# Kernel optimization log

Measured on AMD Instinct MI355X. Metric: run time of the kernel, lower is better.

Reference implementation:

```python
import jax, jax.numpy as jnp
import numpy as np

E = 512   # fusion_dim
H = 8     # num_heads
HD = E // H
NC = 6

def _ln(x, g, b, eps=1e-5):
    m = jnp.mean(x, axis=-1, keepdims=True)
    v = jnp.mean((x - m) ** 2, axis=-1, keepdims=True)
    return (x - m) * jax.lax.rsqrt(v + eps) * g + b

def _lin(x, w, b):
    # torch nn.Linear: w is (out, in)
    return x @ w.T + b

def setup_inputs() -> dict:
    key = jax.random.key(0)
    ks = iter(jax.random.split(key, 32))
    B = 16384
    d = {
        'rgb':  jax.random.normal(next(ks), (B, 768), jnp.float32),
        'pose': jax.random.normal(next(ks), (B, 640), jnp.float32),
        'flow': jax.random.normal(next(ks), (B, 1024), jnp.float32),
    }
    def W(k, shape):
        return jax.random.normal(k, shape, jnp.float32) * 0.02
    # projection branches: Linear + LayerNorm
    d['rgb_w'] = W(next(ks), (E, 768));  d['rgb_b'] = jnp.zeros((E,))
    d['rgb_g'] = jnp.ones((E,));         d['rgb_beta'] = jnp.zeros((E,))
    d['pose_w'] = W(next(ks), (E, 640)); d['pose_b'] = jnp.zeros((E,))
    d['pose_g'] = jnp.ones((E,));        d['pose_beta'] = jnp.zeros((E,))
    d['flow_w'] = W(next(ks), (E, 1024)); d['flow_b'] = jnp.zeros((E,))
    d['flow_g'] = jnp.ones((E,));        d['flow_beta'] = jnp.zeros((E,))
    # MultiheadAttention packed qkv + out proj (torch layout)
    d['in_w'] = W(next(ks), (3 * E, E)); d['in_b'] = jnp.zeros((3 * E,))
    d['out_w'] = W(next(ks), (E, E));    d['out_b'] = jnp.zeros((E,))
    # gate MLP
    d['gw1'] = W(next(ks), (E, 3 * E)); d['gb1'] = jnp.zeros((E,))
    d['gw2'] = W(next(ks), (3, E));     d['gb2'] = jnp.zeros((3,))
    # classifier
    d['cw1'] = W(next(ks), (E // 2, E)); d['cb1'] = jnp.zeros((E // 2,))
    d['cg'] = jnp.ones((E // 2,));       d['cbeta'] = jnp.zeros((E // 2,))
    d['cw2'] = W(next(ks), (NC, E // 2)); d['cb2'] = jnp.zeros((NC,))
    return d

def _forward(rgb, pose, flow, rgb_w, rgb_b, rgb_g, rgb_beta,
             pose_w, pose_b, pose_g, pose_beta,
             flow_w, flow_b, flow_g, flow_beta,
             in_w, in_b, out_w, out_b,
             gw1, gb1, gw2, gb2,
             cw1, cb1, cg, cbeta, cw2, cb2):
    # per-modality projection: Linear -> LN -> ReLU (dropout = identity, eval mode)
    r = jax.nn.relu(_ln(_lin(rgb, rgb_w, rgb_b), rgb_g, rgb_beta))
    p = jax.nn.relu(_ln(_lin(pose, pose_w, pose_b), pose_g, pose_beta))
    f = jax.nn.relu(_ln(_lin(flow, flow_w, flow_b), flow_g, flow_beta))
    stacked = jnp.stack([r, p, f], axis=1)                 # (B, 3, E)
    # self-attention over the 3 modality tokens
    qkv = stacked @ in_w.T + in_b                          # (B, 3, 3E)
    q, k, v = jnp.split(qkv, 3, axis=-1)
    B = stacked.shape[0]
    q = q.reshape(B, 3, H, HD); k = k.reshape(B, 3, H, HD); v = v.reshape(B, 3, H, HD)
    scores = jnp.einsum('bqhd,bkhd->bhqk', q, k) / np.sqrt(HD).astype(np.float32)
    attn = jax.nn.softmax(scores, axis=-1)
    ctx = jnp.einsum('bhqk,bkhd->bqhd', attn, v).reshape(B, 3, E)
    attended = ctx @ out_w.T + out_b                       # (B, 3, E)
    # gating over concatenated projections
    concat = jnp.concatenate([r, p, f], axis=1)            # (B, 3E)
    gate = jax.nn.softmax(_lin(jax.nn.relu(_lin(concat, gw1, gb1)), gw2, gb2), axis=1)  # (B, 3)
    fused = jnp.einsum('bse,bs->be', attended, gate)       # (B, E)
    # classifier
    h = jax.nn.relu(_ln(_lin(fused, cw1, cb1), cg, cbeta))
    logits = _lin(h, cw2, cb2)                             # (B, NC)
    return logits, gate

def reference(rgb, pose, flow, rgb_w, rgb_b, rgb_g, rgb_beta,
              pose_w, pose_b, pose_g, pose_beta,
              flow_w, flow_b, flow_g, flow_beta,
              in_w, in_b, out_w, out_b,
              gw1, gb1, gw2, gb2,
              cw1, cb1, cg, cbeta, cw2, cb2):
    return _forward(rgb, pose, flow, rgb_w, rgb_b, rgb_g, rgb_beta,
                    pose_w, pose_b, pose_g, pose_beta,
                    flow_w, flow_b, flow_g, flow_beta,
                    in_w, in_b, out_w, out_b,
                    gw1, gb1, gw2, gb2,
                    cw1, cb1, cg, cbeta, cw2, cb2)
```

## Files before the change

### kernel.cpp

```cpp
#include <hip/hip_runtime.h>


typedef unsigned short u16;
typedef __bf16 bf16x8 __attribute__((ext_vector_type(8)));
typedef float f32x4  __attribute__((ext_vector_type(4)));
typedef unsigned short u16x8 __attribute__((ext_vector_type(8)));
typedef unsigned short u16x4 __attribute__((ext_vector_type(4)));

#define BATCH 16384

__device__ __forceinline__ u16 f2b(float f) {
  union { float f; unsigned int u; } c; c.f = f;
  unsigned int u = c.u;
  return (u16)((u + 0x7fffu + ((u >> 16) & 1u)) >> 16);
}
__device__ __forceinline__ float b2f(u16 h) {
  union { unsigned int u; float f; } c; c.u = ((unsigned int)h) << 16;
  return c.f;
}

struct CvtJobs {
  const float* s[7];
  u16* d[7];
  int n4[7];
};

__global__ __launch_bounds__(256) void cvt_multi(CvtJobs J) {
  const int stride = gridDim.x * blockDim.x;
  const int tid = blockIdx.x * blockDim.x + threadIdx.x;
  for (int ji = 0; ji < 7; ++ji) {
    const f32x4* __restrict__ s = (const f32x4*)J.s[ji];
    u16x4* __restrict__ d = (u16x4*)J.d[ji];
    const int n4 = J.n4[ji];
    for (int i = tid; i < n4; i += stride) {
      f32x4 v = s[i];
      u16x4 o;
      #pragma unroll
      for (int c = 0; c < 4; ++c) o[c] = f2b(v[c]);
      d[i] = o;
    }
  }
}

template<int ABF, int EPI, int OUTBF>
__global__ __launch_bounds__(256) void gemm_bt(
    const void* __restrict__ Av, const u16* __restrict__ Bw,
    const float* __restrict__ bias, void* __restrict__ Cv,
    int M, int N, int K)
{
  constexpr int ABYTES = ABF ? 2 : 4;
  constexpr int AROUNDS = ABF ? 2 : 4;
  constexpr int AROWS   = ABF ? 64 : 32;
  __shared__ char As[128 * 32 * ABYTES];
  __shared__ u16 Bs[128 * 32];

  const int t = threadIdx.x;
  const int m0 = blockIdx.y << 7;
  const int n0 = blockIdx.x << 7;
  const int wave = t >> 6, lane = t & 63;
  const int wm = wave & 1, wn = wave >> 1;
  const int lr  = lane & 15;
  const int lk8 = (lane >> 4) << 3;

  const int arow = ABF ? (t >> 2) : (t >> 3);
  const int acol = ABF ? ((t & 3) << 4) : ((t & 7) << 4);
  const int brow = t >> 2;
  const int bcol = (t & 3) << 4;

  f32x4 acc[4][4] = {};

  const size_t rowBytesA = (size_t)K * ABYTES;
  const size_t rowBytesB = (size_t)K * 2;
  const char* Abase = (const char*)Av + (size_t)m0 * rowBytesA + acol;
  const char* Bbase = (const char*)(Bw + (size_t)n0 * K) + bcol;

  for (int k0 = 0; k0 < K; k0 += 32) {
    const char* Ak = Abase + (size_t)k0 * ABYTES;
    const char* Bk = Bbase + (size_t)k0 * 2;
    #pragma unroll
    for (int j = 0; j < AROUNDS; ++j)
      __builtin_amdgcn_global_load_lds(
          (const __attribute__((address_space(1))) void*)(Ak + (size_t)(j * AROWS + arow) * rowBytesA),
          (__attribute__((address_space(3))) void*)(As + (j << 12) + (wave << 10)),
          16, 0, 0);
    #pragma unroll
    for (int j = 0; j < 2; ++j)
      __builtin_amdgcn_global_load_lds(
          (const __attribute__((address_space(1))) void*)(Bk + (size_t)(j * 64 + brow) * rowBytesB),
          (__attribute__((address_space(3))) void*)((char*)Bs + (j << 12) + (wave << 10)),
          16, 0, 0);
    __syncthreads();

    bf16x8 af[4], bfr[4];
    #pragma unroll
    for (int mi = 0; mi < 4; ++mi) {
      const int r = (wm << 6) + (mi << 4) + lr;
      if (ABF) {
        af[mi] = __builtin_bit_cast(bf16x8, *(const u16x8*)&((const u16*)As)[r * 32 + lk8]);
      } else {
        const float* Af = (const float*)As;
        f32x4 lo = *(const f32x4*)&Af[r * 32 + lk8];
        f32x4 hi = *(const f32x4*)&Af[r * 32 + lk8 + 4];
        bf16x8 v;
        #pragma unroll
        for (int d = 0; d < 4; ++d) { v[d] = (__bf16)lo[d]; v[4 + d] = (__bf16)hi[d]; }
        af[mi] = v;
      }
    }
    #pragma unroll
    for (int ni = 0; ni < 4; ++ni) {
      const int r = (wn << 6) + (ni << 4) + lr;
      bfr[ni] = __builtin_bit_cast(bf16x8, *(const u16x8*)&Bs[r * 32 + lk8]);
    }
    #pragma unroll
    for (int mi = 0; mi < 4; ++mi)
      #pragma unroll
      for (int ni = 0; ni < 4; ++ni)
        acc[mi][ni] = __builtin_amdgcn_mfma_f32_16x16x32_bf16(
            af[mi], bfr[ni], acc[mi][ni], 0, 0, 0);
    __syncthreads();
  }

  const int rquad = (lane >> 4) << 2;
  #pragma unroll
  for (int ni = 0; ni < 4; ++ni) {
    const int col = n0 + (wn << 6) + (ni << 4) + lr;
    const float bv = bias[col];
    #pragma unroll
    for (int mi = 0; mi < 4; ++mi) {
      const int rowb = m0 + (wm << 6) + (mi << 4) + rquad;
      #pragma unroll
      for (int r = 0; r < 4; ++r) {
        float v = acc[mi][ni][r] + bv;
        if (EPI == 2) v = fmaxf(v, 0.0f);
        const size_t idx = (size_t)(rowb + r) * N + col;
        if (OUTBF) ((u16*)Cv)[idx] = f2b(v);
        else       ((float*)Cv)[idx] = v;
      }
    }
  }
}

template<int E>
__global__ __launch_bounds__(256) void ln_relu_k(
    const float* __restrict__ src, u16* __restrict__ dst,
    const float* __restrict__ gg, const float* __restrict__ bb,
    int dstStride, int dstOff)
{
  constexpr int V = E >> 6;
  const int wave = threadIdx.x >> 6, lane = threadIdx.x & 63;
  const int row = blockIdx.x * 4 + wave;
  const float* s = src + (size_t)row * E + lane * V;
  float x[V];
  float sum = 0.f, sq = 0.f;
  #pragma unroll
  for (int i = 0; i < V; i += 4) {
    f32x4 v = *(const f32x4*)(s + i);
    #pragma unroll
    for (int c = 0; c < 4; ++c) { float f = v[c]; x[i + c] = f; sum += f; sq += f * f; }
  }
  #pragma unroll
  for (int off = 32; off > 0; off >>= 1) {
    sum += __shfl_xor(sum, off);
    sq  += __shfl_xor(sq,  off);
  }
  const float invE = 1.0f / (float)E;
  const float m = sum * invE;
  const float var = sq * invE - m * m;
  const float rs = rsqrtf(var + 1e-5f);
  u16* d = dst + (size_t)row * dstStride + dstOff + lane * V;
  const float* g = gg + lane * V;
  const float* b = bb + lane * V;
  #pragma unroll
  for (int i = 0; i < V; i += 4) {
    u16x4 o;
    #pragma unroll
    for (int c = 0; c < 4; ++c) {
      float y = (x[i + c] - m) * rs * g[i + c] + b[i + c];
      o[c] = f2b(fmaxf(y, 0.0f));
    }
    *(u16x4*)(d + i) = o;
  }
}

__global__ __launch_bounds__(256) void attn_k(
    const u16* __restrict__ qkv, u16* __restrict__ ctx)
{
  const int gid = blockIdx.x * 256 + threadIdx.x;
  const int b = gid >> 6;
  const int h = (threadIdx.x >> 3) & 7;
  const int ld = threadIdx.x & 7;
  const size_t rb = (size_t)(3 * b) * 1536 + h * 64 + ld * 8;

  float q[3][8], k[3][8], v[3][8];
  #pragma unroll
  for (int i = 0; i < 3; ++i) {
    u16x8 qa = *(const u16x8*)&qkv[rb + (size_t)i * 1536];
    u16x8 ka = *(const u16x8*)&qkv[rb + (size_t)i * 1536 + 512];
    u16x8 va = *(const u16x8*)&qkv[rb + (size_t)i * 1536 + 1024];
    #pragma unroll
    for (int d = 0; d < 8; ++d) { q[i][d] = b2f(qa[d]); k[i][d] = b2f(ka[d]); v[i][d] = b2f(va[d]); }
  }
  float s[9];
  #pragma unroll
  for (int i = 0; i < 3; ++i)
    #pragma unroll
    for (int j = 0; j < 3; ++j) {
      float a = 0.f;
      #pragma unroll
      for (int d = 0; d < 8; ++d) a += q[i][d] * k[j][d];
      s[i * 3 + j] = a;
    }
  #pragma unroll
  for (int m = 1; m < 8; m <<= 1)
    #pragma unroll
    for (int e = 0; e < 9; ++e) s[e] += __shfl_xor(s[e], m);

  const float sc = 0.125f;
  #pragma unroll
  for (int i = 0; i < 3; ++i) {
    const float a0 = s[i * 3 + 0] * sc, a1 = s[i * 3 + 1] * sc, a2 = s[i * 3 + 2] * sc;
    const float mx = fmaxf(a0, fmaxf(a1, a2));
    float e0 = __expf(a0 - mx), e1 = __expf(a1 - mx), e2 = __expf(a2 - mx);
    const float inv = 1.0f / (e0 + e1 + e2);
    e0 *= inv; e1 *= inv; e2 *= inv;
    u16x8 o;
    #pragma unroll
    for (int d = 0; d < 8; ++d)
      o[d] = f2b(e0 * v[0][d] + e1 * v[1][d] + e2 * v[2][d]);
    *(u16x8*)&ctx[(size_t)(3 * b + i) * 512 + h * 64 + ld * 8] = o;
  }
}

__global__ __launch_bounds__(256) void gate_fuse_k(
    const u16* __restrict__ gateh, const float* __restrict__ gw2,
    const float* __restrict__ gb2, const u16* __restrict__ att,
    float* __restrict__ gate_out, u16* __restrict__ fused)
{
  const int wave = threadIdx.x >> 6, lane = threadIdx.x & 63;
  const int b = blockIdx.x * 4 + wave;
  float x[8];
  u16x8 xa = *(const u16x8*)&gateh[(size_t)b * 512 + lane * 8];
  #pragma unroll
  for (int d = 0; d < 8; ++d) x[d] = b2f(xa[d]);
  float s[3] = {0.f, 0.f, 0.f};
  #pragma unroll
  for (int j = 0; j < 3; ++j) {
    const float* w = gw2 + j * 512 + lane * 8;
    #pragma unroll
    for (int d = 0; d < 8; ++d) s[j] += x[d] * w[d];
  }
  #pragma unroll
  for (int m = 1; m < 64; m <<= 1)
    #pragma unroll
    for (int j = 0; j < 3; ++j) s[j] += __shfl_xor(s[j], m);
  #pragma unroll
  for (int j = 0; j < 3; ++j) s[j] += gb2[j];
  const float mx = fmaxf(s[0], fmaxf(s[1], s[2]));
  float g0 = __expf(s[0] - mx), g1 = __expf(s[1] - mx), g2 = __expf(s[2] - mx);
  const float inv = 1.0f / (g0 + g1 + g2);
  g0 *= inv; g1 *= inv; g2 *= inv;
  if (lane == 0) { gate_out[b * 3 + 0] = g0; gate_out[b * 3 + 1] = g1; gate_out[b * 3 + 2] = g2; }
  float o[8] = {};
  const float gw[3] = {g0, g1, g2};
  #pragma unroll
  for (int j = 0; j < 3; ++j) {
    u16x8 aa = *(const u16x8*)&att[(size_t)(3 * b + j) * 512 + lane * 8];
    #pragma unroll
    for (int d = 0; d < 8; ++d) o[d] += gw[j] * b2f(aa[d]);
  }
  u16x8 ov;
  #pragma unroll
  for (int d = 0; d < 8; ++d) ov[d] = f2b(o[d]);
  *(u16x8*)&fused[(size_t)b * 512 + lane * 8] = ov;
}

__global__ __launch_bounds__(256) void cls2_k(
    const u16* __restrict__ hh, const float* __restrict__ cw2,
    const float* __restrict__ cb2, float* __restrict__ logits)
{
  const int wave = threadIdx.x >> 6, lane = threadIdx.x & 63;
  const int b = blockIdx.x * 4 + wave;
  float x[4];
  u16x4 xa = *(const u16x4*)&hh[(size_t)b * 256 + lane * 4];
  #pragma unroll
  for (int d = 0; d < 4; ++d) x[d] = b2f(xa[d]);
  float s[6] = {};
  #pragma unroll
  for (int j = 0; j < 6; ++j) {
    const float* w = cw2 + j * 256 + lane * 4;
    #pragma unroll
    for (int d = 0; d < 4; ++d) s[j] += x[d] * w[d];
  }
  #pragma unroll
  for (int m = 1; m < 64; m <<= 1)
    #pragma unroll
    for (int j = 0; j < 6; ++j) s[j] += __shfl_xor(s[j], m);
  if (lane < 6) logits[(size_t)b * 6 + lane] = s[lane] + cb2[lane];
}

extern "C" void kernel_launch(void* const* d_in, const int* in_sizes, int n_in,
                              void* d_out, int out_size, void* d_ws, size_t ws_size,
                              hipStream_t stream) {
  const float* rgb       = (const float*)d_in[0];
  const float* pose      = (const float*)d_in[1];
  const float* flow      = (const float*)d_in[2];
  const float* rgb_w     = (const float*)d_in[3];
  const float* rgb_b     = (const float*)d_in[4];
  const float* rgb_g     = (const float*)d_in[5];
  const float* rgb_beta  = (const float*)d_in[6];
  const float* pose_w    = (const float*)d_in[7];
  const float* pose_b    = (const float*)d_in[8];
  const float* pose_g    = (const float*)d_in[9];
  const float* pose_beta = (const float*)d_in[10];
  const float* flow_w    = (const float*)d_in[11];
  const float* flow_b    = (const float*)d_in[12];
  const float* flow_g    = (const float*)d_in[13];
  const float* flow_beta = (const float*)d_in[14];
  const float* in_w      = (const float*)d_in[15];
  const float* in_b      = (const float*)d_in[16];
  const float* out_w     = (const float*)d_in[17];
  const float* out_b     = (const float*)d_in[18];
  const float* gw1       = (const float*)d_in[19];
  const float* gb1       = (const float*)d_in[20];
  const float* gw2       = (const float*)d_in[21];
  const float* gb2       = (const float*)d_in[22];
  const float* cw1       = (const float*)d_in[23];
  const float* cb1       = (const float*)d_in[24];
  const float* cg        = (const float*)d_in[25];
  const float* cbeta     = (const float*)d_in[26];
  const float* cw2       = (const float*)d_in[27];
  const float* cb2       = (const float*)d_in[28];

  float* logits_out = (float*)d_out;
  float* gate_out   = (float*)d_out + (size_t)BATCH * 6;

  char* ws = (char*)d_ws;
  u16* w_rgb  = (u16*)(ws + 0);
  u16* w_pose = (u16*)(ws + 786432);
  u16* w_flow = (u16*)(ws + 1441792);
  u16* w_in   = (u16*)(ws + 2490368);
  u16* w_out  = (u16*)(ws + 4063232);
  u16* w_g1   = (u16*)(ws + 4587520);
  u16* w_c1   = (u16*)(ws + 6160384);
  char* rpfB = ws + 6422528;
  char* ctxB = ws + 56754176;
  char* r1B  = ws + 107085824;

  u16*   rpf      = (u16*)rpfB;
  u16*   att      = (u16*)rpfB;
  u16*   ctx      = (u16*)ctxB;
  float* cls_tmp  = (float*)ctxB;
  u16*   h_bf     = (u16*)(ctxB + 16777216);
  float* proj_tmp = (float*)r1B;
  u16*   qkv_buf  = (u16*)r1B;
  u16*   gateh    = (u16*)r1B;
  u16*   fusedb   = (u16*)(r1B + 16777216);

  CvtJobs J;
  const float* srcs[7] = {rgb_w, pose_w, flow_w, in_w, out_w, gw1, cw1};
  u16* dsts[7] = {w_rgb, w_pose, w_flow, w_in, w_out, w_g1, w_c1};
  int ns[7] = {512 * 768, 512 * 640, 512 * 1024, 1536 * 512, 512 * 512, 512 * 1536, 256 * 512};
  for (int i = 0; i < 7; ++i) { J.s[i] = srcs[i]; J.d[i] = dsts[i]; J.n4[i] = ns[i] / 4; }
  cvt_multi<<<512, 256, 0, stream>>>(J);

  dim3 blk(256);
  gemm_bt<0, 1, 0><<<dim3(4, BATCH / 128), blk, 0, stream>>>(rgb, w_rgb, rgb_b, proj_tmp, BATCH, 512, 768);
  ln_relu_k<512><<<BATCH / 4, blk, 0, stream>>>(proj_tmp, rpf, rgb_g, rgb_beta, 1536, 0);
  gemm_bt<0, 1, 0><<<dim3(4, BATCH / 128), blk, 0, stream>>>(pose, w_pose, pose_b, proj_tmp, BATCH, 512, 640);
  ln_relu_k<512><<<BATCH / 4, blk, 0, stream>>>(proj_tmp, rpf, pose_g, pose_beta, 1536, 512);
  gemm_bt<0, 1, 0><<<dim3(4, BATCH / 128), blk, 0, stream>>>(flow, w_flow, flow_b, proj_tmp, BATCH, 512, 1024);
  ln_relu_k<512><<<BATCH / 4, blk, 0, stream>>>(proj_tmp, rpf, flow_g, flow_beta, 1536, 1024);

  for (int c = 0; c < 4; ++c) {
    const u16* a_chunk = rpf + (size_t)c * 4096 * 1536;
    u16* ctx_chunk = ctx + (size_t)c * 4096 * 3 * 512;
    gemm_bt<1, 1, 1><<<dim3(12, 3 * 4096 / 128), blk, 0, stream>>>(
        a_chunk, w_in, in_b, qkv_buf, 3 * 4096, 1536, 512);
    attn_k<<<4096 / 4, blk, 0, stream>>>(qkv_buf, ctx_chunk);
  }

  gemm_bt<1, 2, 1><<<dim3(4, BATCH / 128), blk, 0, stream>>>(rpf, w_g1, gb1, gateh, BATCH, 512, 1536);

  gemm_bt<1, 1, 1><<<dim3(4, 3 * BATCH / 128), blk, 0, stream>>>(ctx, w_out, out_b, att, 3 * BATCH, 512, 512);

  gate_fuse_k<<<BATCH / 4, blk, 0, stream>>>(gateh, gw2, gb2, att, gate_out, fusedb);

  gemm_bt<1, 1, 0><<<dim3(2, BATCH / 128), blk, 0, stream>>>(fusedb, w_c1, cb1, cls_tmp, BATCH, 256, 512);
  ln_relu_k<256><<<BATCH / 4, blk, 0, stream>>>(cls_tmp, h_bf, cg, cbeta, 256, 0);
  cls2_k<<<BATCH / 4, blk, 0, stream>>>(h_bf, cw2, cb2, logits_out);

  (void)in_sizes; (void)n_in; (void)out_size; (void)ws_size;
}
```

Before: 682.8 us.

## Double-buffer GEMM with 64-row tiles, bf16 intermediates, merged projection LayerNorm

Replaces the 128x128 GEMM with a 64x128 tile kernel that double-buffers LDS and prefetches the next K-slice before computing the current one, which also drops one barrier per iteration. The smaller M tile doubles the number of blocks. Projection GEMMs now write bf16 straight into a strided 1536-wide buffer, and a single three-modality LayerNorm kernel replaces three separate LN launches. The classifier intermediate is also stored as bf16. This cuts launches and fp32 intermediate traffic, at the cost of LayerNorm statistics being computed from bf16-rounded values and less data reuse per tile.

Measured after the change: 704.4 us. +3.2%, slower.

```diff
diff --git a/kernel.cpp b/kernel.cpp
--- a/kernel.cpp
+++ b/kernel.cpp
@@ -43,22 +43,23 @@
 }
 
 template<int ABF, int EPI, int OUTBF>
-__global__ __launch_bounds__(256) void gemm_bt(
+__global__ __launch_bounds__(256) void gemm64(
     const void* __restrict__ Av, const u16* __restrict__ Bw,
     const float* __restrict__ bias, void* __restrict__ Cv,
-    int M, int N, int K)
-{
-  constexpr int ABYTES = ABF ? 2 : 4;
-  constexpr int AROUNDS = ABF ? 2 : 4;
-  constexpr int AROWS   = ABF ? 64 : 32;
-  __shared__ char As[128 * 32 * ABYTES];
-  __shared__ u16 Bs[128 * 32];
+    int M, int N, int K, int ldc, int coff)
+{
+  constexpr int ABYTES  = ABF ? 2 : 4;
+  constexpr int ATILE   = 64 * 32 * ABYTES;
+  constexpr int AROUNDS = ATILE / 4096;
+  constexpr int AR_ROWS = ABF ? 64 : 32;
+  __shared__ __align__(16) char As[2][ATILE];
+  __shared__ __align__(16) u16  Bs[2][128 * 32];
 
   const int t = threadIdx.x;
-  const int m0 = blockIdx.y << 7;
+  const int m0 = blockIdx.y << 6;
   const int n0 = blockIdx.x << 7;
   const int wave = t >> 6, lane = t & 63;
-  const int wm = wave & 1, wn = wave >> 1;
+  const int nbase = wave << 5;
   const int lr  = lane & 15;
   const int lk8 = (lane >> 4) << 3;
 
@@ -67,38 +68,45 @@
   const int brow = t >> 2;
   const int bcol = (t & 3) << 4;
 
-  f32x4 acc[4][4] = {};
+  f32x4 acc[4][2] = {};
 
   const size_t rowBytesA = (size_t)K * ABYTES;
   const size_t rowBytesB = (size_t)K * 2;
   const char* Abase = (const char*)Av + (size_t)m0 * rowBytesA + acol;
   const char* Bbase = (const char*)(Bw + (size_t)n0 * K) + bcol;
 
-  for (int k0 = 0; k0 < K; k0 += 32) {
-    const char* Ak = Abase + (size_t)k0 * ABYTES;
-    const char* Bk = Bbase + (size_t)k0 * 2;
+  auto stage = [&](int s, int buf) {
+    const char* Ak = Abase + (size_t)s * (32 * ABYTES);
     #pragma unroll
     for (int j = 0; j < AROUNDS; ++j)
       __builtin_amdgcn_global_load_lds(
-          (const __attribute__((address_space(1))) void*)(Ak + (size_t)(j * AROWS + arow) * rowBytesA),
-          (__attribute__((address_space(3))) void*)(As + (j << 12) + (wave << 10)),
+          (const __attribute__((address_space(1))) void*)(Ak + (size_t)(j * AR_ROWS + arow) * rowBytesA),
+          (__attribute__((address_space(3))) void*)(&As[buf][(j << 12) + (wave << 10)]),
           16, 0, 0);
+    const char* Bk = Bbase + (size_t)s * 64;
     #pragma unroll
     for (int j = 0; j < 2; ++j)
       __builtin_amdgcn_global_load_lds(
           (const __attribute__((address_space(1))) void*)(Bk + (size_t)(j * 64 + brow) * rowBytesB),
-          (__attribute__((address_space(3))) void*)((char*)Bs + (j << 12) + (wave << 10)),
+          (__attribute__((address_space(3))) void*)((char*)Bs[buf] + (j << 12) + (wave << 10)),
           16, 0, 0);
+  };
+
+  const int nsteps = K >> 5;
+  stage(0, 0);
+  for (int s = 0; s < nsteps; ++s) {
+    const int cur = s & 1;
     __syncthreads();
-
-    bf16x8 af[4], bfr[4];
+    if (s + 1 < nsteps) stage(s + 1, cur ^ 1);
+
+    bf16x8 af[4], bf[2];
     #pragma unroll
     for (int mi = 0; mi < 4; ++mi) {
-      const int r = (wm << 6) + (mi << 4) + lr;
+      const int r = (mi << 4) + lr;
       if (ABF) {
-        af[mi] = __builtin_bit_cast(bf16x8, *(const u16x8*)&((const u16*)As)[r * 32 + lk8]);
+        af[mi] = __builtin_bit_cast(bf16x8, *(const u16x8*)&((const u16*)As[cur])[r * 32 + lk8]);
       } else {
-        const float* Af = (const float*)As;
+        const float* Af = (const float*)As[cur];
         f32x4 lo = *(const f32x4*)&Af[r * 32 + lk8];
         f32x4 hi = *(const f32x4*)&Af[r * 32 + lk8 + 4];
         bf16x8 v;
@@ -108,32 +116,31 @@
       }
     }
     #pragma unroll
-    for (int ni = 0; ni < 4; ++ni) {
-      const int r = (wn << 6) + (ni << 4) + lr;
-      bfr[ni] = __builtin_bit_cast(bf16x8, *(const u16x8*)&Bs[r * 32 + lk8]);
+    for (int ni = 0; ni < 2; ++ni) {
+      const int r = nbase + (ni << 4) + lr;
+      bf[ni] = __builtin_bit_cast(bf16x8, *(const u16x8*)&Bs[cur][r * 32 + lk8]);
     }
     #pragma unroll
     for (int mi = 0; mi < 4; ++mi)
       #pragma unroll
-      for (int ni = 0; ni < 4; ++ni)
+      for (int ni = 0; ni < 2; ++ni)
         acc[mi][ni] = __builtin_amdgcn_mfma_f32_16x16x32_bf16(
-            af[mi], bfr[ni], acc[mi][ni], 0, 0, 0);
-    __syncthreads();
+            af[mi], bf[ni], acc[mi][ni], 0, 0, 0);
   }
 
   const int rquad = (lane >> 4) << 2;
   #pragma unroll
-  for (int ni = 0; ni < 4; ++ni) {
-    const int col = n0 + (wn << 6) + (ni << 4) + lr;
+  for (int ni = 0; ni < 2; ++ni) {
+    const int col = n0 + nbase + (ni << 4) + lr;
     const float bv = bias[col];
     #pragma unroll
     for (int mi = 0; mi < 4; ++mi) {
-      const int rowb = m0 + (wm << 6) + (mi << 4) + rquad;
+      const int rowb = m0 + (mi << 4) + rquad;
       #pragma unroll
       for (int r = 0; r < 4; ++r) {
         float v = acc[mi][ni][r] + bv;
         if (EPI == 2) v = fmaxf(v, 0.0f);
-        const size_t idx = (size_t)(rowb + r) * N + col;
+        const size_t idx = (size_t)(rowb + r) * ldc + coff + col;
         if (OUTBF) ((u16*)Cv)[idx] = f2b(v);
         else       ((float*)Cv)[idx] = v;
       }
@@ -141,23 +148,53 @@
   }
 }
 
+__global__ __launch_bounds__(384) void ln3_k(
+    const u16* __restrict__ raw, u16* __restrict__ dst,
+    const float* __restrict__ g0, const float* __restrict__ b0,
+    const float* __restrict__ g1, const float* __restrict__ b1,
+    const float* __restrict__ g2, const float* __restrict__ b2)
+{
+  const int wave = threadIdx.x >> 6, lane = threadIdx.x & 63;
+  const int m = wave % 3;
+  const int b = blockIdx.x * 2 + wave / 3;
+  const size_t off = (size_t)b * 1536 + m * 512 + lane * 8;
+  u16x8 xa = *(const u16x8*)&raw[off];
+  float x[8];
+  float sum = 0.f, sq = 0.f;
+  #pragma unroll
+  for (int d = 0; d < 8; ++d) { float f = b2f(xa[d]); x[d] = f; sum += f; sq += f * f; }
+  #pragma unroll
+  for (int o = 32; o > 0; o >>= 1) { sum += __shfl_xor(sum, o); sq += __shfl_xor(sq, o); }
+  const float mean = sum * (1.0f / 512.0f);
+  const float var = sq * (1.0f / 512.0f) - mean * mean;
+  const float rs = rsqrtf(var + 1e-5f);
+  const float* g = (m == 0) ? g0 : (m == 1) ? g1 : g2;
+  const float* bb = (m == 0) ? b0 : (m == 1) ? b1 : b2;
+  u16x8 o;
+  #pragma unroll
+  for (int d = 0; d < 8; ++d) {
+    float y = (x[d] - mean) * rs * g[lane * 8 + d] + bb[lane * 8 + d];
+    o[d] = f2b(fmaxf(y, 0.0f));
+  }
+  *(u16x8*)&dst[off] = o;
+}
+
 template<int E>
 __global__ __launch_bounds__(256) void ln_relu_k(
-    const float* __restrict__ src, u16* __restrict__ dst,
-    const float* __restrict__ gg, const float* __restrict__ bb,
-    int dstStride, int dstOff)
+    const u16* __restrict__ src, u16* __restrict__ dst,
+    const float* __restrict__ gg, const float* __restrict__ bb)
 {
   constexpr int V = E >> 6;
   const int wave = threadIdx.x >> 6, lane = threadIdx.x & 63;
   const int row = blockIdx.x * 4 + wave;
-  const float* s = src + (size_t)row * E + lane * V;
+  const u16* s = src + (size_t)row * E + lane * V;
   float x[V];
   float sum = 0.f, sq = 0.f;
   #pragma unroll
   for (int i = 0; i < V; i += 4) {
-    f32x4 v = *(const f32x4*)(s + i);
-    #pragma unroll
-    for (int c = 0; c < 4; ++c) { float f = v[c]; x[i + c] = f; sum += f; sq += f * f; }
+    u16x4 v = *(const u16x4*)(s + i);
+    #pragma unroll
+    for (int c = 0; c < 4; ++c) { float f = b2f(v[c]); x[i + c] = f; sum += f; sq += f * f; }
   }
   #pragma unroll
   for (int off = 32; off > 0; off >>= 1) {
@@ -168,7 +205,7 @@
   const float m = sum * invE;
   const float var = sq * invE - m * m;
   const float rs = rsqrtf(var + 1e-5f);
-  u16* d = dst + (size_t)row * dstStride + dstOff + lane * V;
+  u16* d = dst + (size_t)row * E + lane * V;
   const float* g = gg + lane * V;
   const float* b = bb + lane * V;
   #pragma unroll
@@ -349,10 +386,10 @@
 
   u16*   rpf      = (u16*)rpfB;
   u16*   att      = (u16*)rpfB;
+  u16*   raw      = (u16*)ctxB;
   u16*   ctx      = (u16*)ctxB;
-  float* cls_tmp  = (float*)ctxB;
-  u16*   h_bf     = (u16*)(ctxB + 16777216);
-  float* proj_tmp = (float*)r1B;
+  u16*   cls_tmp  = (u16*)ctxB;
+  u16*   h_bf     = (u16*)(ctxB + 8388608);
   u16*   qkv_buf  = (u16*)r1B;
   u16*   gateh    = (u16*)r1B;
   u16*   fusedb   = (u16*)(r1B + 16777216);
@@ -365,29 +402,27 @@
   cvt_multi<<<512, 256, 0, stream>>>(J);
 
   dim3 blk(256);
-  gemm_bt<0, 1, 0><<<dim3(4, BATCH / 128), blk, 0, stream>>>(rgb, w_rgb, rgb_b, proj_tmp, BATCH, 512, 768);
-  ln_relu_k<512><<<BATCH / 4, blk, 0, stream>>>(proj_tmp, rpf, rgb_g, rgb_beta, 1536, 0);
-  gemm_bt<0, 1, 0><<<dim3(4, BATCH / 128), blk, 0, stream>>>(pose, w_pose, pose_b, proj_tmp, BATCH, 512, 640);
-  ln_relu_k<512><<<BATCH / 4, blk, 0, stream>>>(proj_tmp, rpf, pose_g, pose_beta, 1536, 512);
-  gemm_bt<0, 1, 0><<<dim3(4, BATCH / 128), blk, 0, stream>>>(flow, w_flow, flow_b, proj_tmp, BATCH, 512, 1024);
-  ln_relu_k<512><<<BATCH / 4, blk, 0, stream>>>(proj_tmp, rpf, flow_g, flow_beta, 1536, 1024);
+  gemm64<0, 1, 1><<<dim3(4, BATCH / 64), blk, 0, stream>>>(rgb,  w_rgb,  rgb_b,  raw, BATCH, 512, 768,  1536, 0);
+  gemm64<0, 1, 1><<<dim3(4, BATCH / 64), blk, 0, stream>>>(pose, w_pose, pose_b, raw, BATCH, 512, 640,  1536, 512);
+  gemm64<0, 1, 1><<<dim3(4, BATCH / 64), blk, 0, stream>>>(flow, w_flow, flow_b, raw, BATCH, 512, 1024, 1536, 1024);
+  ln3_k<<<BATCH / 2, dim3(384), 0, stream>>>(raw, rpf, rgb_g, rgb_beta, pose_g, pose_beta, flow_g, flow_beta);
 
   for (int c = 0; c < 4; ++c) {
     const u16* a_chunk = rpf + (size_t)c * 4096 * 1536;
     u16* ctx_chunk = ctx + (size_t)c * 4096 * 3 * 512;
-    gemm_bt<1, 1, 1><<<dim3(12, 3 * 4096 / 128), blk, 0, stream>>>(
-        a_chunk, w_in, in_b, qkv_buf, 3 * 4096, 1536, 512);
+    gemm64<1, 1, 1><<<dim3(12, 3 * 4096 / 64), blk, 0, stream>>>(
+        a_chunk, w_in, in_b, qkv_buf, 3 * 4096, 1536, 512, 1536, 0);
     attn_k<<<4096 / 4, blk, 0, stream>>>(qkv_buf, ctx_chunk);
   }
 
-  gemm_bt<1, 2, 1><<<dim3(4, BATCH / 128), blk, 0, stream>>>(rpf, w_g1, gb1, gateh, BATCH, 512, 1536);
-
-  gemm_bt<1, 1, 1><<<dim3(4, 3 * BATCH / 128), blk, 0, stream>>>(ctx, w_out, out_b, att, 3 * BATCH, 512, 512);
+  gemm64<1, 2, 1><<<dim3(4, BATCH / 64), blk, 0, stream>>>(rpf, w_g1, gb1, gateh, BATCH, 512, 1536, 512, 0);
+
+  gemm64<1, 1, 1><<<dim3(4, 3 * BATCH / 64), blk, 0, stream>>>(ctx, w_out, out_b, att, 3 * BATCH, 512, 512, 512, 0);
 
   gate_fuse_k<<<BATCH / 4, blk, 0, stream>>>(gateh, gw2, gb2, att, gate_out, fusedb);
 
-  gemm_bt<1, 1, 0><<<dim3(2, BATCH / 128), blk, 0, stream>>>(fusedb, w_c1, cb1, cls_tmp, BATCH, 256, 512);
-  ln_relu_k<256><<<BATCH / 4, blk, 0, stream>>>(cls_tmp, h_bf, cg, cbeta, 256, 0);
+  gemm64<1, 1, 1><<<dim3(2, BATCH / 64), blk, 0, stream>>>(fusedb, w_c1, cb1, cls_tmp, BATCH, 256, 512, 256, 0);
+  ln_relu_k<256><<<BATCH / 4, blk, 0, stream>>>(cls_tmp, h_bf, cg, cbeta);
   cls2_k<<<BATCH / 4, blk, 0, stream>>>(h_bf, cw2, cb2, logits_out);
 
   (void)in_sizes; (void)n_in; (void)out_size; (void)ws_size;
```
